# Performance work log

Measured on AMD Instinct MI355X. Metric: run time of the kernel, lower is better.

## Reference

```python
import jax, jax.numpy as jnp
import numpy as np

B, IN, H = 8192, 1024, 1024


def setup_inputs() -> dict:
    key = jax.random.key(0)
    ks = jax.random.split(key, 6)
    s = 1.0 / np.sqrt(H)
    return {
        "incoming": jax.random.normal(ks[0], (B, IN), dtype=jnp.float32),
        "state": jax.random.normal(ks[1], (2, B, H), dtype=jnp.float32),
        "Wx": jax.random.normal(ks[2], (4 * H, IN), dtype=jnp.float32) * s,
        "bx": jax.random.normal(ks[3], (4 * H,), dtype=jnp.float32) * s,
        "Wh": jax.random.normal(ks[4], (4 * H, H), dtype=jnp.float32) * s,
        "bh": jax.random.normal(ks[5], (4 * H,), dtype=jnp.float32) * s,
    }


def reference(incoming, state, Wx, bx, Wh, bh):
    # Fused form of 8 Linear layers: gates stacked in (i, f, g, o) order.
    h_prev, c_prev = state[0], state[1]
    gates = (jnp.einsum('bi,gi->bg', incoming, Wx) + bx
             + jnp.einsum('bh,gh->bg', h_prev, Wh) + bh)  # [B, 4H]
    i_g, f_g, g_g, o_g = jnp.split(gates, 4, axis=-1)
    i = jax.nn.sigmoid(i_g)
    f = jax.nn.sigmoid(f_g)
    g = jnp.tanh(g_g)
    o = jax.nn.sigmoid(o_g)
    new_c = f * c_prev + i * g
    new_h = o * jnp.tanh(new_c)
    # output == new_h; return stacked (new_h, new_c) as [2, B, H]
    return jnp.stack([new_h, new_c])
```

## Files before the change

### kernel.cpp

```cpp
#include <hip/hip_runtime.h>
#include <hip/hip_bf16.h>


#define B_DIM 8192
#define H_DIM 1024
#define BH (8192 * 1024)
#define K2 2048

typedef __attribute__((ext_vector_type(4))) float f32x4;
typedef __attribute__((ext_vector_type(8))) __bf16 bf16x8;
typedef __attribute__((ext_vector_type(8))) unsigned short ushort8;

static __device__ __forceinline__ unsigned short f2bf(float f) {
    return __builtin_bit_cast(unsigned short, (__bf16)f);
}
static __device__ __forceinline__ float sigf(float x) {
    return 1.0f / (1.0f + __expf(-x));
}
static __device__ __forceinline__ float tanhft(float x) {
    float e = __expf(2.0f * x);
    return (e - 1.0f) / (e + 1.0f);
}
static __device__ __forceinline__ void gload16(const void* g, void* l) {
    __builtin_amdgcn_global_load_lds(
        (const __attribute__((address_space(1))) unsigned int*)g,
        (__attribute__((address_space(3))) unsigned int*)l, 16, 0, 0);
}
static __device__ __forceinline__ ushort8 cvt8(const float* src) {
    const float4 u = ((const float4*)src)[0];
    const float4 v = ((const float4*)src)[1];
    ushort8 o;
    o[0] = f2bf(u.x); o[1] = f2bf(u.y); o[2] = f2bf(u.z); o[3] = f2bf(u.w);
    o[4] = f2bf(v.x); o[5] = f2bf(v.y); o[6] = f2bf(v.z); o[7] = f2bf(v.w);
    return o;
}

__global__ __launch_bounds__(256) void conv_kernel(
    const float* __restrict__ x, const float* __restrict__ h,
    const float* __restrict__ Wx, const float* __restrict__ Wh,
    unsigned short* __restrict__ A, unsigned short* __restrict__ W)
{
    const int bidx = blockIdx.x;
    if (bidx < 8192) {
        const int id = bidx * 256 + threadIdx.x;
        const int base = id * 8;
        const int b = base >> 11;
        const int k = base & 2047;
        const float* src = (k < 1024) ? (x + (size_t)b * 1024 + k)
                                      : (h + (size_t)b * 1024 + (k - 1024));
        *(ushort8*)(A + base) = cvt8(src);
    } else {
        const int id = (bidx - 8192) * 256 + threadIdx.x;
        const int base = id * 8;
        const int n = base >> 11;
        const int k = base & 2047;
        const int jb = n >> 8, wn = (n >> 6) & 3, g = (n >> 4) & 3, jj = n & 15;
        const int srow = (g << 10) + (jb << 6) + (wn << 4) + jj;
        const float* src = (k < 1024) ? (Wx + (size_t)srow * 1024 + k)
                                      : (Wh + (size_t)srow * 1024 + (k - 1024));
        *(ushort8*)(W + base) = cvt8(src);
    }
}

__global__ __launch_bounds__(512, 2) void lstm_gemm8(
    const unsigned short* __restrict__ Abf, const unsigned short* __restrict__ Wbf,
    const float* __restrict__ bx, const float* __restrict__ bh,
    const float* __restrict__ cprev, float* __restrict__ out)
{
    extern __shared__ unsigned short lds[];

    const int tid = threadIdx.x;
    const int lane = tid & 63;
    const int wv = tid >> 6;
    const int wm = wv >> 2;
    const int wn = wv & 3;
    const int q = lane >> 4, c = lane & 15;

    const int bid = blockIdx.x;
    const int xcd = bid & 7;
    const int idx = bid >> 3;
    const int jb  = xcd * 2 + (idx & 1);
    const int bb  = idx >> 1;
    const int b0 = bb * 256;

    const unsigned short* Ab = Abf + (size_t)b0 * K2;
    const unsigned short* Wb = Wbf + (size_t)(jb * 256) * K2;

    const size_t ssg = (size_t)(tid >> 3) * K2
                     + (size_t)(((tid & 7) ^ ((tid >> 3) & 7)) * 8);
    const unsigned sbase = (unsigned)(tid & 448) * 8;

    const unsigned arow = (unsigned)(wm * 128 + c) * 64;
    const unsigned brow = 16384u + (unsigned)(wn * 64 + c) * 64;
    const unsigned cach = (unsigned)((q ^ (c & 7)) << 3);

    f32x4 acc[8][4];
#pragma unroll
    for (int m = 0; m < 8; ++m)
#pragma unroll
        for (int g = 0; g < 4; ++g) acc[m][g] = f32x4{0.f, 0.f, 0.f, 0.f};

    bf16x8 av[4], bv[4];

#define STG(BUF, ISB, QA, T) do {                                              \
    const unsigned short* _s = (ISB) ? Wb : Ab;                                \
    gload16(_s + ssg + (size_t)(QA) * 64 * K2 + (size_t)((T) & 31) * 64,       \
            &lds[(BUF) * 32768 + (ISB) * 16384 + (QA) * 4096 + sbase]);        \
} while (0)

#define LOADA(BUF, KS, MH) do {                                                \
    const unsigned short* _p = lds + (BUF) * 32768 + (MH) * 4096 + arow        \
                             + (cach ^ ((KS) * 32));                           \
    av[0] = *(const bf16x8*)(_p);                                              \
    av[1] = *(const bf16x8*)(_p + 1024);                                       \
    av[2] = *(const bf16x8*)(_p + 2048);                                       \
    av[3] = *(const bf16x8*)(_p + 3072);                                       \
} while (0)

#define LOADB(BUF, KS) do {                                                    \
    const unsigned short* _p = lds + (BUF) * 32768 + brow                      \
                             + (cach ^ ((KS) * 32));                           \
    bv[0] = *(const bf16x8*)(_p);                                              \
    bv[1] = *(const bf16x8*)(_p + 1024);                                       \
    bv[2] = *(const bf16x8*)(_p + 2048);                                       \
    bv[3] = *(const bf16x8*)(_p + 3072);                                       \
} while (0)

#define MFMA16(MH) do {                                                        \
    __builtin_amdgcn_s_setprio(1);                                             \
    _Pragma("unroll")                                                          \
    for (int _i = 0; _i < 4; ++_i)                                             \
        _Pragma("unroll")                                                      \
        for (int _g = 0; _g < 4; ++_g)                                         \
            acc[(MH) * 4 + _i][_g] = __builtin_amdgcn_mfma_f32_16x16x32_bf16(  \
                av[_i], bv[_g], acc[(MH) * 4 + _i][_g], 0, 0, 0);              \
    __builtin_amdgcn_s_setprio(0);                                             \
} while (0)

#define BAR()  __builtin_amdgcn_s_barrier()
#define WVM2() asm volatile("s_waitcnt vmcnt(2)" ::: "memory")

#define TILE(BUF, T1) do {                                                     \
    LOADA(BUF, 0, 0); LOADB(BUF, 0);                                           \
    STG((BUF) ^ 1, 1, 0, T1); STG((BUF) ^ 1, 1, 1, T1);                        \
    MFMA16(0); WVM2(); BAR();                                                  \
    LOADA(BUF, 0, 1);                                                          \
    STG((BUF) ^ 1, 1, 2, T1); STG((BUF) ^ 1, 1, 3, T1);                        \
    MFMA16(1); BAR();                                                          \
    LOADA(BUF, 1, 0); LOADB(BUF, 1);                                           \
    STG((BUF) ^ 1, 0, 0, T1); STG((BUF) ^ 1, 0, 2, T1);                        \
    MFMA16(0); BAR();                                                          \
    LOADA(BUF, 1, 1);                                                          \
    STG((BUF) ^ 1, 0, 1, T1); STG((BUF) ^ 1, 0, 3, T1);                        \
    MFMA16(1); WVM2(); BAR();                                                  \
} while (0)

    STG(0, 1, 0, 0); STG(0, 1, 1, 0); STG(0, 1, 2, 0); STG(0, 1, 3, 0);
    STG(0, 0, 0, 0); STG(0, 0, 2, 0); STG(0, 0, 1, 0); STG(0, 0, 3, 0);
    WVM2();
    BAR();

    for (int u = 0; u < 32; u += 2) {
        TILE(0, u + 1);
        TILE(1, u + 2);
    }

#undef TILE
#undef STG
#undef LOADA
#undef LOADB
#undef MFMA16

    const int j = jb * 64 + wn * 16 + c;
    const float bI = bx[j] + bh[j];
    const float bF = bx[1024 + j] + bh[1024 + j];
    const float bG = bx[2048 + j] + bh[2048 + j];
    const float bO = bx[3072 + j] + bh[3072 + j];
#pragma unroll
    for (int mt = 0; mt < 8; ++mt) {
#pragma unroll
        for (int rr = 0; rr < 4; ++rr) {
            const int row = b0 + wm * 128 + mt * 16 + q * 4 + rr;
            const size_t off = (size_t)row * 1024 + j;
            const float iv = sigf(acc[mt][0][rr] + bI);
            const float fv = sigf(acc[mt][1][rr] + bF);
            const float gv = tanhft(acc[mt][2][rr] + bG);
            const float ov = sigf(acc[mt][3][rr] + bO);
            const float cp = cprev[off];
            const float nc = fv * cp + iv * gv;
            out[off] = ov * tanhft(nc);
            out[BH + off] = nc;
        }
    }
}

__global__ __launch_bounds__(256) void lstm_fallback(
    const float* __restrict__ incoming, const float* __restrict__ state,
    const float* __restrict__ Wx, const float* __restrict__ bx,
    const float* __restrict__ Wh, const float* __restrict__ bh,
    float* __restrict__ out)
{
    __shared__ unsigned short lA[128 * 64];
    __shared__ unsigned short lW[128 * 64];
    const int t = threadIdx.x;
    const int lane = t & 63;
    const int wv = t >> 6;
    const int q = lane >> 4;
    const int c = lane & 15;
    const int j0 = blockIdx.x * 32;
    const int b0 = blockIdx.y * 128;
    const float* hprev = state;
    const float* cprev = state + (size_t)BH;

    f32x4 acc[2][8];
#pragma unroll
    for (int mt = 0; mt < 2; ++mt)
#pragma unroll
        for (int nt = 0; nt < 8; ++nt)
            acc[mt][nt] = f32x4{0.f, 0.f, 0.f, 0.f};

    const int sr = t >> 3;
    const int sk8 = t & 7;

    for (int it = 0; it < 32; ++it) {
        const bool first = (it < 16);
        const float* As = first ? incoming : hprev;
        const float* Ws = first ? Wx : Wh;
        const int kk = first ? it * 64 : it * 64 - 1024;
#pragma unroll
        for (int i = 0; i < 4; ++i) {
            const int r = i * 32 + sr;
            *(ushort8*)&lA[r * 64 + ((sk8 ^ (r & 7)) * 8)] =
                cvt8(As + (size_t)(b0 + r) * 1024 + kk + sk8 * 8);
        }
#pragma unroll
        for (int i = 0; i < 4; ++i) {
            const int n = i * 32 + sr;
            const int grow = ((n >> 5) << 10) + j0 + (n & 31);
            *(ushort8*)&lW[n * 64 + ((sk8 ^ (n & 7)) * 8)] =
                cvt8(Ws + (size_t)grow * 1024 + kk + sk8 * 8);
        }
        __syncthreads();
#pragma unroll
        for (int ks = 0; ks < 2; ++ks) {
            const int k8a = ks * 4 + q;
            bf16x8 av[2], bv[8];
#pragma unroll
            for (int mt = 0; mt < 2; ++mt) {
                const int r = wv * 32 + mt * 16 + c;
                av[mt] = *(const bf16x8*)&lA[r * 64 + ((k8a ^ (r & 7)) * 8)];
            }
#pragma unroll
            for (int nt = 0; nt < 8; ++nt) {
                const int n = nt * 16 + c;
                bv[nt] = *(const bf16x8*)&lW[n * 64 + ((k8a ^ (n & 7)) * 8)];
            }
#pragma unroll
            for (int mt = 0; mt < 2; ++mt)
#pragma unroll
                for (int nt = 0; nt < 8; ++nt)
                    acc[mt][nt] = __builtin_amdgcn_mfma_f32_16x16x32_bf16(
                        av[mt], bv[nt], acc[mt][nt], 0, 0, 0);
        }
        __syncthreads();
    }

    const int b0r = b0 + wv * 32;
#pragma unroll
    for (int jt = 0; jt < 2; ++jt) {
        const int j = j0 + jt * 16 + c;
        const float bI = bx[j] + bh[j];
        const float bF = bx[1024 + j] + bh[1024 + j];
        const float bG = bx[2048 + j] + bh[2048 + j];
        const float bO = bx[3072 + j] + bh[3072 + j];
#pragma unroll
        for (int mt = 0; mt < 2; ++mt) {
#pragma unroll
            for (int rr = 0; rr < 4; ++rr) {
                const int row = b0r + mt * 16 + q * 4 + rr;
                const size_t off = (size_t)row * 1024 + j;
                const float iv = sigf(acc[mt][0 + jt][rr] + bI);
                const float fv = sigf(acc[mt][2 + jt][rr] + bF);
                const float gv = tanhft(acc[mt][4 + jt][rr] + bG);
                const float ov = sigf(acc[mt][6 + jt][rr] + bO);
                const float cp = cprev[off];
                const float nc = fv * cp + iv * gv;
                out[off] = ov * tanhft(nc);
                out[BH + off] = nc;
            }
        }
    }
}

extern "C" void kernel_launch(void* const* d_in, const int* in_sizes, int n_in,
                              void* d_out, int out_size, void* d_ws, size_t ws_size,
                              hipStream_t stream) {
    const float* incoming = (const float*)d_in[0];
    const float* state    = (const float*)d_in[1];
    const float* Wx       = (const float*)d_in[2];
    const float* bx       = (const float*)d_in[3];
    const float* Wh       = (const float*)d_in[4];
    const float* bh       = (const float*)d_in[5];
    float* out = (float*)d_out;

    const float* hprev = state;
    const float* cprev = state + (size_t)BH;

    const size_t A_bytes = (size_t)B_DIM * K2 * 2;
    const size_t W_bytes = (size_t)4 * H_DIM * K2 * 2;

    if (ws_size >= A_bytes + W_bytes) {
        unsigned short* Abf = (unsigned short*)d_ws;
        unsigned short* Wbf = (unsigned short*)((char*)d_ws + A_bytes);
        conv_kernel<<<dim3(12288), dim3(256), 0, stream>>>(
            incoming, hprev, Wx, Wh, Abf, Wbf);
        (void)hipFuncSetAttribute((const void*)lstm_gemm8,
                                  hipFuncAttributeMaxDynamicSharedMemorySize, 131072);
        lstm_gemm8<<<dim3(512), dim3(512), 131072, stream>>>(
            Abf, Wbf, bx, bh, cprev, out);
    } else {
        dim3 grid(H_DIM / 32, B_DIM / 128);
        lstm_fallback<<<grid, dim3(256), 0, stream>>>(
            incoming, state, Wx, bx, Wh, bh, out);
    }
}
```

Baseline: 159.8 us.

## Load B operand straight from global into registers, stage only A in LDS

The weight (B) tile is no longer staged through LDS. Each wave now loads its own B fragments directly from global memory into double-buffered registers one tile ahead, so only the A tile goes through LDS and the dynamic LDS allocation halves. The inner tile schedule is also simplified to one barrier per K tile, with a single vmcnt wait. This removes the LDS traffic and barriers for B, but adds register pressure from the extra bvA/bvB buffers. Each B element is now fetched from global/L2 once per wave instead of being shared through LDS, which can raise global load traffic.

```diff
diff --git a/kernel.cpp b/kernel.cpp
--- a/kernel.cpp
+++ b/kernel.cpp
@@ -62,7 +62,7 @@
     }
 }
 
-__global__ __launch_bounds__(512, 2) void lstm_gemm8(
+__global__ __launch_bounds__(512, 2) void lstm_gemm_br(
     const unsigned short* __restrict__ Abf, const unsigned short* __restrict__ Wbf,
     const float* __restrict__ bx, const float* __restrict__ bh,
     const float* __restrict__ cprev, float* __restrict__ out)
@@ -91,25 +91,38 @@
     const unsigned sbase = (unsigned)(tid & 448) * 8;
 
     const unsigned arow = (unsigned)(wm * 128 + c) * 64;
-    const unsigned brow = 16384u + (unsigned)(wn * 64 + c) * 64;
     const unsigned cach = (unsigned)((q ^ (c & 7)) << 3);
 
+    const unsigned short* Wbp = Wb + (size_t)(wn * 64 + c) * K2 + (size_t)q * 8;
+
     f32x4 acc[8][4];
 #pragma unroll
     for (int m = 0; m < 8; ++m)
 #pragma unroll
         for (int g = 0; g < 4; ++g) acc[m][g] = f32x4{0.f, 0.f, 0.f, 0.f};
 
-    bf16x8 av[4], bv[4];
-
-#define STG(BUF, ISB, QA, T) do {                                              \
-    const unsigned short* _s = (ISB) ? Wb : Ab;                                \
-    gload16(_s + ssg + (size_t)(QA) * 64 * K2 + (size_t)((T) & 31) * 64,       \
-            &lds[(BUF) * 32768 + (ISB) * 16384 + (QA) * 4096 + sbase]);        \
+    bf16x8 av[4];
+    bf16x8 bvA[2][4], bvB[2][4];
+
+#define STG(BUF, QA, T) do {                                                   \
+    gload16(Ab + ssg + (size_t)(QA) * 64 * K2 + (size_t)((T) & 31) * 64,       \
+            &lds[(BUF) * 16384 + (QA) * 4096 + sbase]);                        \
+} while (0)
+
+#define LDB(DST, T) do {                                                       \
+    const unsigned short* _w = Wbp + (size_t)((T) & 31) * 64;                  \
+    DST[0][0] = *(const bf16x8*)(_w);                                          \
+    DST[1][0] = *(const bf16x8*)(_w + 32);                                     \
+    DST[0][1] = *(const bf16x8*)(_w + (size_t)16 * K2);                        \
+    DST[1][1] = *(const bf16x8*)(_w + (size_t)16 * K2 + 32);                   \
+    DST[0][2] = *(const bf16x8*)(_w + (size_t)32 * K2);                        \
+    DST[1][2] = *(const bf16x8*)(_w + (size_t)32 * K2 + 32);                   \
+    DST[0][3] = *(const bf16x8*)(_w + (size_t)48 * K2);                        \
+    DST[1][3] = *(const bf16x8*)(_w + (size_t)48 * K2 + 32);                   \
 } while (0)
 
 #define LOADA(BUF, KS, MH) do {                                                \
-    const unsigned short* _p = lds + (BUF) * 32768 + (MH) * 4096 + arow        \
+    const unsigned short* _p = lds + (BUF) * 16384 + (MH) * 4096 + arow        \
                              + (cach ^ ((KS) * 32));                           \
     av[0] = *(const bf16x8*)(_p);                                              \
     av[1] = *(const bf16x8*)(_p + 1024);                                       \
@@ -117,58 +130,48 @@
     av[3] = *(const bf16x8*)(_p + 3072);                                       \
 } while (0)
 
-#define LOADB(BUF, KS) do {                                                    \
-    const unsigned short* _p = lds + (BUF) * 32768 + brow                      \
-                             + (cach ^ ((KS) * 32));                           \
-    bv[0] = *(const bf16x8*)(_p);                                              \
-    bv[1] = *(const bf16x8*)(_p + 1024);                                       \
-    bv[2] = *(const bf16x8*)(_p + 2048);                                       \
-    bv[3] = *(const bf16x8*)(_p + 3072);                                       \
-} while (0)
-
-#define MFMA16(MH) do {                                                        \
+#define MFMA16(MH, BV, KS) do {                                                \
     __builtin_amdgcn_s_setprio(1);                                             \
     _Pragma("unroll")                                                          \
     for (int _i = 0; _i < 4; ++_i)                                             \
         _Pragma("unroll")                                                      \
         for (int _g = 0; _g < 4; ++_g)                                         \
             acc[(MH) * 4 + _i][_g] = __builtin_amdgcn_mfma_f32_16x16x32_bf16(  \
-                av[_i], bv[_g], acc[(MH) * 4 + _i][_g], 0, 0, 0);              \
+                av[_i], BV[KS][_g], acc[(MH) * 4 + _i][_g], 0, 0, 0);          \
     __builtin_amdgcn_s_setprio(0);                                             \
 } while (0)
 
 #define BAR()  __builtin_amdgcn_s_barrier()
-#define WVM2() asm volatile("s_waitcnt vmcnt(2)" ::: "memory")
-
-#define TILE(BUF, T1) do {                                                     \
-    LOADA(BUF, 0, 0); LOADB(BUF, 0);                                           \
-    STG((BUF) ^ 1, 1, 0, T1); STG((BUF) ^ 1, 1, 1, T1);                        \
-    MFMA16(0); WVM2(); BAR();                                                  \
-    LOADA(BUF, 0, 1);                                                          \
-    STG((BUF) ^ 1, 1, 2, T1); STG((BUF) ^ 1, 1, 3, T1);                        \
-    MFMA16(1); BAR();                                                          \
-    LOADA(BUF, 1, 0); LOADB(BUF, 1);                                           \
-    STG((BUF) ^ 1, 0, 0, T1); STG((BUF) ^ 1, 0, 2, T1);                        \
-    MFMA16(0); BAR();                                                          \
-    LOADA(BUF, 1, 1);                                                          \
-    STG((BUF) ^ 1, 0, 1, T1); STG((BUF) ^ 1, 0, 3, T1);                        \
-    MFMA16(1); WVM2(); BAR();                                                  \
-} while (0)
-
-    STG(0, 1, 0, 0); STG(0, 1, 1, 0); STG(0, 1, 2, 0); STG(0, 1, 3, 0);
-    STG(0, 0, 0, 0); STG(0, 0, 2, 0); STG(0, 0, 1, 0); STG(0, 0, 3, 0);
-    WVM2();
+#define SCHB() __builtin_amdgcn_sched_barrier(0)
+#define WVM8() asm volatile("s_waitcnt vmcnt(8)" ::: "memory")
+
+#define TILE(BUF, BVC, BVN, T1) do {                                           \
+    STG((BUF) ^ 1, 0, T1); STG((BUF) ^ 1, 1, T1);                              \
+    STG((BUF) ^ 1, 2, T1); STG((BUF) ^ 1, 3, T1);                              \
+    SCHB();                                                                    \
+    LDB(BVN, T1);                                                              \
+    LOADA(BUF, 0, 0); MFMA16(0, BVC, 0);                                       \
+    LOADA(BUF, 0, 1); MFMA16(1, BVC, 0);                                       \
+    LOADA(BUF, 1, 0); MFMA16(0, BVC, 1);                                       \
+    LOADA(BUF, 1, 1); MFMA16(1, BVC, 1);                                       \
+    WVM8(); BAR();                                                             \
+} while (0)
+
+    STG(0, 0, 0); STG(0, 1, 0); STG(0, 2, 0); STG(0, 3, 0);
+    SCHB();
+    LDB(bvA, 0);
+    WVM8();
     BAR();
 
     for (int u = 0; u < 32; u += 2) {
-        TILE(0, u + 1);
-        TILE(1, u + 2);
+        TILE(0, bvA, bvB, u + 1);
+        TILE(1, bvB, bvA, u + 2);
     }
 
 #undef TILE
 #undef STG
+#undef LDB
 #undef LOADA
-#undef LOADB
 #undef MFMA16
 
     const int j = jb * 64 + wn * 16 + c;
@@ -314,9 +317,9 @@
         unsigned short* Wbf = (unsigned short*)((char*)d_ws + A_bytes);
         conv_kernel<<<dim3(12288), dim3(256), 0, stream>>>(
             incoming, hprev, Wx, Wh, Abf, Wbf);
-        (void)hipFuncSetAttribute((const void*)lstm_gemm8,
-                                  hipFuncAttributeMaxDynamicSharedMemorySize, 131072);
-        lstm_gemm8<<<dim3(512), dim3(512), 131072, stream>>>(
+        (void)hipFuncSetAttribute((const void*)lstm_gemm_br,
+                                  hipFuncAttributeMaxDynamicSharedMemorySize, 65536);
+        lstm_gemm_br<<<dim3(512), dim3(512), 65536, stream>>>(
             Abf, Wbf, bx, bh, cprev, out);
     } else {
         dim3 grid(H_DIM / 32, B_DIM / 128);
```

After: 212.5 us. 1.33x slower.
